# Kernel tuning notes

Hardware: AMD Instinct MI355X
Metric: run time of the kernel (lower is better)

The kernel has to match this reference:

```python
import jax, jax.numpy as jnp
import numpy as np
import math

N, S, T, E, H = 2, 2048, 2048, 1024, 16
HD = E // H  # head_dim = 64


def setup_inputs() -> dict:
    key = jax.random.key(0)
    ks = jax.random.split(key, 11)
    scale = 1.0 / math.sqrt(E)
    inp = {
        "query": jax.random.normal(ks[0], (N, S, E), jnp.float32),
        "key": jax.random.normal(ks[1], (N, T, E), jnp.float32),
        "value": jax.random.normal(ks[2], (N, T, E), jnp.float32),
        "Wq": jax.random.normal(ks[3], (E, E), jnp.float32) * scale,
        "bq": jnp.zeros((E,), jnp.float32),
        "Wk": jax.random.normal(ks[4], (E, E), jnp.float32) * scale,
        "bk": jnp.zeros((E,), jnp.float32),
        "Wv": jax.random.normal(ks[5], (E, E), jnp.float32) * scale,
        "bv": jnp.zeros((E,), jnp.float32),
        "Wo": jax.random.normal(ks[6], (E, E), jnp.float32) * scale,
        "bo": jnp.zeros((E,), jnp.float32),
    }
    return inp


def reference(query, key, value, Wq, bq, Wk, bk, Wv, bv, Wo, bo):
    # QKV projections, then split heads: [N, S, E] -> [N, H, S, HD]
    q = (query @ Wq + bq).reshape(N, S, H, HD).transpose(0, 2, 1, 3)
    k = (key @ Wk + bk).reshape(N, T, H, HD).transpose(0, 2, 1, 3)
    v = (value @ Wv + bv).reshape(N, T, H, HD).transpose(0, 2, 1, 3)
    # scaled dot-product attention scores [N, H, S, T]
    scores = jnp.einsum('nhse,nhte->nhst', q, k) / math.sqrt(HD)
    attn = jax.nn.softmax(scores, axis=-1)
    # dropout is identity in eval mode
    out = jnp.einsum('nhst,nhte->nhse', attn, v)  # [N, H, S, HD]
    out = out.transpose(0, 2, 1, 3).reshape(N, S, E)
    return out @ Wo + bo
```

## Files before the change

kernel.cpp:

```cpp
#include <hip/hip_runtime.h>
#include <hip/hip_bf16.h>

typedef __bf16 bf16x8 __attribute__((ext_vector_type(8)));
typedef __bf16 bf16x4 __attribute__((ext_vector_type(4)));
typedef float  f32x4  __attribute__((ext_vector_type(4)));
typedef float  f32x16 __attribute__((ext_vector_type(16)));
typedef unsigned int u32x4 __attribute__((ext_vector_type(4)));

#define MFMA16(a, b, c) __builtin_amdgcn_mfma_f32_16x16x32_bf16((a), (b), (c), 0, 0, 0)
#define MFMA32(a, b, c) __builtin_amdgcn_mfma_f32_32x32x16_bf16((a), (b), (c), 0, 0, 0)

constexpr int SEQ = 2048, EMB = 1024, NHEAD = 16, HD = 64;
constexpr float SSCALE = 0.18033688f;

__device__ __forceinline__ void glds16(const void* g, void* l) {
    __builtin_amdgcn_global_load_lds(
        (const __attribute__((address_space(1))) void*)g,
        (__attribute__((address_space(3))) void*)l, 16, 0, 0);
}

__global__ __launch_bounds__(256)
void prep(const float* __restrict__ W0, const float* __restrict__ W1,
          const float* __restrict__ W2, const float* __restrict__ W3,
          __bf16* __restrict__ T0, __bf16* __restrict__ T1,
          __bf16* __restrict__ T2, __bf16* __restrict__ T3,
          const float* __restrict__ X0, const float* __restrict__ X1,
          const float* __restrict__ X2, __bf16* __restrict__ Y0,
          __bf16* __restrict__ Y1, __bf16* __restrict__ Y2)
{
    __shared__ float tile[32][33];
    const int z = blockIdx.z;
    if (z < 4) {
        const float* W = (z==0) ? W0 : (z==1) ? W1 : (z==2) ? W2 : W3;
        __bf16*      T = (z==0) ? T0 : (z==1) ? T1 : (z==2) ? T2 : T3;
        const float s = (z == 0) ? SSCALE : 1.0f;
        const int kb = blockIdx.x * 32, nb = blockIdx.y * 32;
        const int c = threadIdx.x & 31, r0 = threadIdx.x >> 5;
#pragma unroll
        for (int i = 0; i < 4; ++i)
            tile[r0 + 8*i][c] = W[(size_t)(kb + r0 + 8*i)*1024 + nb + c];
        __syncthreads();
#pragma unroll
        for (int i = 0; i < 4; ++i)
            T[(size_t)(nb + r0 + 8*i)*1024 + kb + c] = (__bf16)(tile[c][r0 + 8*i] * s);
    } else {
        const float* X = (z==4) ? X0 : (z==5) ? X1 : X2;
        __bf16*      Y = (z==4) ? Y0 : (z==5) ? Y1 : Y2;
        const size_t base =
            ((size_t)(blockIdx.y * 32 + blockIdx.x) * 256 + threadIdx.x) * 16;
#pragma unroll
        for (int j = 0; j < 2; ++j) {
            const float4* s4 = (const float4*)(X + base + j*8);
            float4 f0 = s4[0], f1 = s4[1];
            bf16x8 v;
            v[0]=(__bf16)f0.x; v[1]=(__bf16)f0.y; v[2]=(__bf16)f0.z; v[3]=(__bf16)f0.w;
            v[4]=(__bf16)f1.x; v[5]=(__bf16)f1.y; v[6]=(__bf16)f1.z; v[7]=(__bf16)f1.w;
            *(bf16x8*)(Y + base + j*8) = v;
        }
    }
}

struct GArg { const __bf16* A; const __bf16* Bt; const float* bias; void* C;
              int mode; int kbase; int kcount; float bscale; };
struct GArgs3 { GArg a[3]; };

__global__ __launch_bounds__(256)
void gemmk(GArgs3 args)
{
    const int lin = blockIdx.x + (blockIdx.y << 5) + (blockIdx.z << 8);
    const int nid = (lin & 7) * 96 + (lin >> 3);
    const int gz = nid >> 8, rem = nid & 255;
    const int bm = rem >> 3, bn = rem & 7;
    const GArg g = args.a[gz];
    __shared__ __attribute__((aligned(16))) __bf16 As[128*64];
    __shared__ __attribute__((aligned(16))) __bf16 Bs[128*64];
    const int tid = threadIdx.x, lane = tid & 63, wave = tid >> 6;
    const int wm = wave >> 1, wn = wave & 1;
    const int quad = lane >> 4, l16 = lane & 15;

    f32x4 acc[4][4] = {};

    for (int kt = 0; kt < g.kcount; ++kt) {
        const int k0 = g.kbase + kt*64;
        __syncthreads();
#pragma unroll
        for (int j = 0; j < 4; ++j) {
            const int ci = j*256 + tid;
            const int row = ci >> 3, cg = ((ci & 7) ^ (row & 7)) * 8;
            glds16(g.A + (size_t)(bm*128 + row)*1024 + k0 + cg,
                   &As[(j*256 + wave*64)*8]);
        }
#pragma unroll
        for (int j = 0; j < 4; ++j) {
            const int ci = j*256 + tid;
            const int row = ci >> 3, cg = ((ci & 7) ^ (row & 7)) * 8;
            glds16(g.Bt + (size_t)(bn*128 + row)*1024 + k0 + cg,
                   &Bs[(j*256 + wave*64)*8]);
        }
        __syncthreads();
#pragma unroll
        for (int ks = 0; ks < 2; ++ks) {
            const int kc = ks*4 + quad;
            bf16x8 af[4], bfr[4];
#pragma unroll
            for (int mt = 0; mt < 4; ++mt) {
                const int ar = wm*64 + mt*16 + l16;
                af[mt] = *(const bf16x8*)&As[ar*64 + (kc ^ (ar & 7))*8];
            }
#pragma unroll
            for (int nt = 0; nt < 4; ++nt) {
                const int br = wn*64 + nt*16 + l16;
                bfr[nt] = *(const bf16x8*)&Bs[br*64 + (kc ^ (br & 7))*8];
            }
#pragma unroll
            for (int mt = 0; mt < 4; ++mt)
#pragma unroll
                for (int nt = 0; nt < 4; ++nt)
                    acc[mt][nt] = MFMA16(af[mt], bfr[nt], acc[mt][nt]);
        }
    }

#pragma unroll
    for (int nt = 0; nt < 4; ++nt) {
        const int n = bn*128 + wn*64 + nt*16 + l16;
        const float bvs = (g.bias ? g.bias[n] : 0.f) * g.bscale;
#pragma unroll
        for (int mt = 0; mt < 4; ++mt) {
            const int mbase = bm*128 + wm*64 + mt*16 + quad*4;
            f32x4 v = acc[mt][nt];
            if (g.mode == 0) {
                __bf16* C = (__bf16*)g.C;
                const int h = n >> 6, d = n & 63;
#pragma unroll
                for (int r = 0; r < 4; ++r) {
                    const int m = mbase + r;
                    const int nb = m >> 11, s = m & 2047;
                    C[(size_t)(nb*NHEAD + h)*(SEQ*HD) + (size_t)s*HD + d] = (__bf16)(v[r] + bvs);
                }
            } else {
                __bf16* C = (__bf16*)g.C;
                const int h = n >> 6, d = n & 63;
                const int nb = mbase >> 11, s = mbase & 2047;
                const int tg = (s >> 2) & 7;
                const int pg = (tg & 4) | ((tg & 1) << 1) | ((tg & 2) >> 1);
                const int sp = (s & ~31) | (pg << 2);
                bf16x4 o;
#pragma unroll
                for (int r = 0; r < 4; ++r) o[r] = (__bf16)(v[r] + bvs);
                *(bf16x4*)&C[(size_t)(nb*NHEAD + h)*(SEQ*HD) + (size_t)d*SEQ + sp] = o;
            }
        }
    }
}

__global__ __launch_bounds__(256)
void gemmo(const __bf16* __restrict__ A, const __bf16* __restrict__ Bt,
           const float* __restrict__ bias, float* __restrict__ C)
{
    const int lin = blockIdx.x + (blockIdx.y << 6);
    const int nid = (lin & 7) * 64 + (lin >> 3);
    const int bm = nid >> 3, bn = nid & 7;
    __shared__ __attribute__((aligned(16))) __bf16 As[64*64];
    __shared__ __attribute__((aligned(16))) __bf16 Bs[128*64];
    const int tid = threadIdx.x, lane = tid & 63, wave = tid >> 6;
    const int quad = lane >> 4, l16 = lane & 15;

    f32x4 acc[4][2] = {};

    for (int k0 = 0; k0 < 1024; k0 += 64) {
        __syncthreads();
#pragma unroll
        for (int j = 0; j < 2; ++j) {
            const int ci = j*256 + tid;
            const int row = ci >> 3, cg = ((ci & 7) ^ (row & 7)) * 8;
            glds16(A + (size_t)(bm*64 + row)*1024 + k0 + cg,
                   &As[(j*256 + wave*64)*8]);
        }
#pragma unroll
        for (int j = 0; j < 4; ++j) {
            const int ci = j*256 + tid;
            const int row = ci >> 3, cg = ((ci & 7) ^ (row & 7)) * 8;
            glds16(Bt + (size_t)(bn*128 + row)*1024 + k0 + cg,
                   &Bs[(j*256 + wave*64)*8]);
        }
        __syncthreads();
#pragma unroll
        for (int ks = 0; ks < 2; ++ks) {
            const int kc = ks*4 + quad;
            bf16x8 af[4], bfr[2];
#pragma unroll
            for (int mt = 0; mt < 4; ++mt) {
                const int ar = mt*16 + l16;
                af[mt] = *(const bf16x8*)&As[ar*64 + (kc ^ (ar & 7))*8];
            }
#pragma unroll
            for (int nt = 0; nt < 2; ++nt) {
                const int br = wave*32 + nt*16 + l16;
                bfr[nt] = *(const bf16x8*)&Bs[br*64 + (kc ^ (br & 7))*8];
            }
#pragma unroll
            for (int mt = 0; mt < 4; ++mt)
#pragma unroll
                for (int nt = 0; nt < 2; ++nt)
                    acc[mt][nt] = MFMA16(af[mt], bfr[nt], acc[mt][nt]);
        }
    }
#pragma unroll
    for (int nt = 0; nt < 2; ++nt) {
        const int n = bn*128 + wave*32 + nt*16 + l16;
        const float bv = bias[n];
#pragma unroll
        for (int mt = 0; mt < 4; ++mt) {
            const int mbase = bm*64 + mt*16 + quad*4;
            f32x4 v = acc[mt][nt];
#pragma unroll
            for (int r = 0; r < 4; ++r)
                C[(size_t)(mbase + r)*1024 + n] = v[r] + bv;
        }
    }
}

__global__ __launch_bounds__(512, 2)
void attn32(const __bf16* __restrict__ qg, const __bf16* __restrict__ kg,
            const __bf16* __restrict__ vg, __bf16* __restrict__ Og)
{
    __shared__ __attribute__((aligned(16))) char smem[64*1024];
    float* Xch = (float*)smem;

    const int tid = threadIdx.x, lane = tid & 63, wave = tid >> 6;
    const int w4 = wave & 3, grp = wave >> 2;
    const int l32 = lane & 31, half = lane >> 5;
    const int nh = blockIdx.y;
    const int q0 = blockIdx.x * 128;
    const __bf16* qb = qg + (size_t)nh * (SEQ*HD);
    const __bf16* kb = kg + (size_t)nh * (SEQ*HD);
    const __bf16* vb = vg + (size_t)nh * (SEQ*HD);

    bf16x8 qf[4];
#pragma unroll
    for (int ks = 0; ks < 4; ++ks)
        qf[ks] = *(const bf16x8*)(qb + (size_t)(q0 + w4*32 + l32)*HD + ks*16 + half*8);

    bf16x8 vone;
#pragma unroll
    for (int i = 0; i < 8; ++i) vone[i] = (__bf16)1.0f;

    f32x16 oacc[2] = {};
    f32x16 osum = {};

    const int cK0 = tid, rK0 = cK0 >> 3;
    const int cK1 = 512 + tid, rK1 = cK1 >> 3;
    const __bf16* kp0 = kb + (size_t)rK0*HD + ((cK0 & 7) ^ (rK0 & 7)) * 8;
    const __bf16* kp1 = kb + (size_t)rK1*HD + ((cK1 & 7) ^ (rK1 & 7)) * 8;
    const int cV0 = tid, rV0 = cV0 >> 4, pV0 = cV0 & 15;
    const int cV1 = 512 + tid, rV1 = cV1 >> 4, pV1 = cV1 & 15;
    const __bf16* vp0 = vb + (size_t)rV0*SEQ + (((pV0 & ~7) | ((pV0 & 7) ^ (rV0 & 7))) * 8);
    const __bf16* vp1 = vb + (size_t)rV1*SEQ + (((pV1 & ~7) | ((pV1 & 7) ^ (rV1 & 7))) * 8);

    auto stage = [&](int b) {
        char* Kd = smem + b * 16384;
        char* Vd = smem + 32768 + b * 16384;
        glds16(kp0, Kd + wave*1024);
        glds16(kp1, Kd + 8192 + wave*1024);
        glds16(vp0, Vd + wave*1024);
        glds16(vp1, Vd + 8192 + wave*1024);
        kp0 += 128*HD; kp1 += 128*HD;
        vp0 += 128;    vp1 += 128;
    };

    stage(0);
    int cur = 0;
    for (int it = 0; it < 16; ++it) {
        __syncthreads();
        if (it < 15) stage(cur ^ 1);

        const __bf16* Ks = (const __bf16*)(smem + cur * 16384);
        const __bf16* Vs = (const __bf16*)(smem + 32768 + cur * 16384);

        f32x16 sc[2] = {};
        __builtin_amdgcn_s_setprio(1);
#pragma unroll
        for (int ks = 0; ks < 4; ++ks) {
            const int c = ks*2 + half;
#pragma unroll
            for (int nt = 0; nt < 2; ++nt) {
                const int kr = grp*64 + nt*32 + l32;
                bf16x8 kf = *(const bf16x8*)&Ks[kr*64 + ((c ^ (kr & 7))*8)];
                sc[nt] = MFMA32(kf, qf[ks], sc[nt]);
            }
        }
        __builtin_amdgcn_s_setprio(0);

#pragma unroll
        for (int nt = 0; nt < 2; ++nt)
#pragma unroll
            for (int sub = 0; sub < 2; ++sub) {
                const float e0 = __builtin_amdgcn_exp2f(sc[nt][sub*8 + 0]);
                const float e1 = __builtin_amdgcn_exp2f(sc[nt][sub*8 + 1]);
                const float e2 = __builtin_amdgcn_exp2f(sc[nt][sub*8 + 2]);
                const float e3 = __builtin_amdgcn_exp2f(sc[nt][sub*8 + 3]);
                const float e4 = __builtin_amdgcn_exp2f(sc[nt][sub*8 + 4]);
                const float e5 = __builtin_amdgcn_exp2f(sc[nt][sub*8 + 5]);
                const float e6 = __builtin_amdgcn_exp2f(sc[nt][sub*8 + 6]);
                const float e7 = __builtin_amdgcn_exp2f(sc[nt][sub*8 + 7]);
                u32x4 pk;
                asm("v_cvt_pk_bf16_f32 %0, %1, %2" : "=v"(pk.x) : "v"(e0), "v"(e1));
                asm("v_cvt_pk_bf16_f32 %0, %1, %2" : "=v"(pk.y) : "v"(e2), "v"(e3));
                asm("v_cvt_pk_bf16_f32 %0, %1, %2" : "=v"(pk.z) : "v"(e4), "v"(e5));
                asm("v_cvt_pk_bf16_f32 %0, %1, %2" : "=v"(pk.w) : "v"(e6), "v"(e7));
                const bf16x8 pf = __builtin_bit_cast(bf16x8, pk);
                const int c2 = grp*8 + (nt*2 + sub)*2 + half;
                __builtin_amdgcn_s_setprio(1);
#pragma unroll
                for (int dt = 0; dt < 2; ++dt) {
                    const int vr = dt*32 + l32;
                    const int pos = (c2 & ~7) | ((c2 & 7) ^ (vr & 7));
                    bf16x8 vf = *(const bf16x8*)&Vs[vr*128 + pos*8];
                    oacc[dt] = MFMA32(pf, vf, oacc[dt]);
                }
                osum = MFMA32(pf, vone, osum);
                __builtin_amdgcn_s_setprio(0);
            }
        cur ^= 1;
    }

    __syncthreads();
    if (grp == 1) {
        float* dst = &Xch[((w4*64) + lane) * 48];
#pragma unroll
        for (int i = 0; i < 16; ++i) {
            dst[i]      = oacc[0][i];
            dst[16 + i] = oacc[1][i];
            dst[32 + i] = osum[i];
        }
    }
    __syncthreads();
    if (grp == 0) {
        const float* src = &Xch[((w4*64) + lane) * 48];
#pragma unroll
        for (int i = 0; i < 16; ++i) {
            oacc[0][i] += src[i];
            oacc[1][i] += src[16 + i];
            osum[i]    += src[32 + i];
        }
        const int nb = nh >> 4, h = nh & 15;
#pragma unroll
        for (int reg = 0; reg < 16; ++reg) {
            const int row = (reg & 3) + 8*(reg >> 2) + 4*half;
            const int srow = q0 + w4*32 + row;
            const float inv = 1.0f / osum[reg];
#pragma unroll
            for (int dt = 0; dt < 2; ++dt)
                Og[(size_t)(nb*SEQ + srow)*EMB + h*HD + dt*32 + l32] =
                    (__bf16)(oacc[dt][reg] * inv);
        }
    }
}

extern "C" void kernel_launch(void* const* d_in, const int* in_sizes, int n_in,
                              void* d_out, int out_size, void* d_ws, size_t ws_size,
                              hipStream_t stream)
{
    const float* query = (const float*)d_in[0];
    const float* key_  = (const float*)d_in[1];
    const float* value = (const float*)d_in[2];
    const float* Wq = (const float*)d_in[3];
    const float* bq = (const float*)d_in[4];
    const float* Wk = (const float*)d_in[5];
    const float* bk = (const float*)d_in[6];
    const float* Wv = (const float*)d_in[7];
    const float* bv = (const float*)d_in[8];
    const float* Wo = (const float*)d_in[9];
    const float* bo = (const float*)d_in[10];
    float* out = (float*)d_out;

    constexpr size_t SZW = 1024u*1024u;
    constexpr size_t SZX = 4096u*1024u;
    __bf16* ws  = (__bf16*)d_ws;
    __bf16* WqT = ws;
    __bf16* WkT = WqT + SZW;
    __bf16* WvT = WkT + SZW;
    __bf16* WoT = WvT + SZW;
    __bf16* xv  = WoT + SZW;
    __bf16* qh  = xv + SZX;
    __bf16* kh  = qh + SZX;
    __bf16* vTh = kh + SZX;
    __bf16* xq  = (__bf16*)d_out;
    __bf16* xk  = xq + SZX;
    __bf16* Oh  = xv;

    prep<<<dim3(32, 32, 7), 256, 0, stream>>>(Wq, Wk, Wv, Wo, WqT, WkT, WvT, WoT,
                                              query, key_, value, xq, xk, xv);
    GArgs3 a;
    a.a[0] = { xq, WqT, bq, qh,  0, 0, 16, SSCALE };
    a.a[1] = { xk, WkT, bk, kh,  0, 0, 16, 1.0f };
    a.a[2] = { xv, WvT, bv, vTh, 1, 0, 16, 1.0f };
    gemmk<<<dim3(32, 8, 3), 256, 0, stream>>>(a);
    attn32<<<dim3(16, 32), 512, 0, stream>>>(qh, kh, vTh, Oh);
    gemmo<<<dim3(64, 8), 256, 0, stream>>>(Oh, WoT, bo, out);
}
```

Measured before the change: 211.6 us.

## Software-pipeline QK and PV across iterations, replace ones-MFMA rowsum with scalar sums

```diff
diff --git a/kernel.cpp b/kernel.cpp
--- a/kernel.cpp
+++ b/kernel.cpp
@@ -224,7 +224,7 @@
 void attn32(const __bf16* __restrict__ qg, const __bf16* __restrict__ kg,
             const __bf16* __restrict__ vg, __bf16* __restrict__ Og)
 {
-    __shared__ __attribute__((aligned(16))) char smem[64*1024];
+    __shared__ __attribute__((aligned(16))) char smem[80*1024];
     float* Xch = (float*)smem;
 
     const int tid = threadIdx.x, lane = tid & 63, wave = tid >> 6;
@@ -241,12 +241,8 @@
     for (int ks = 0; ks < 4; ++ks)
         qf[ks] = *(const bf16x8*)(qb + (size_t)(q0 + w4*32 + l32)*HD + ks*16 + half*8);
 
-    bf16x8 vone;
-#pragma unroll
-    for (int i = 0; i < 8; ++i) vone[i] = (__bf16)1.0f;
-
     f32x16 oacc[2] = {};
-    f32x16 osum = {};
+    float psum = 0.0f;
 
     const int cK0 = tid, rK0 = cK0 >> 3;
     const int cK1 = 512 + tid, rK1 = cK1 >> 3;
@@ -257,9 +253,9 @@
     const __bf16* vp0 = vb + (size_t)rV0*SEQ + (((pV0 & ~7) | ((pV0 & 7) ^ (rV0 & 7))) * 8);
     const __bf16* vp1 = vb + (size_t)rV1*SEQ + (((pV1 & ~7) | ((pV1 & 7) ^ (rV1 & 7))) * 8);
 
-    auto stage = [&](int b) {
-        char* Kd = smem + b * 16384;
-        char* Vd = smem + 32768 + b * 16384;
+    auto stage = [&](int t) {
+        char* Kd = smem + (t & 1) * 16384;
+        char* Vd = smem + 32768 + (t % 3) * 16384;
         glds16(kp0, Kd + wave*1024);
         glds16(kp1, Kd + 8192 + wave*1024);
         glds16(vp0, Vd + wave*1024);
@@ -268,16 +264,8 @@
         vp0 += 128;    vp1 += 128;
     };
 
-    stage(0);
-    int cur = 0;
-    for (int it = 0; it < 16; ++it) {
-        __syncthreads();
-        if (it < 15) stage(cur ^ 1);
-
-        const __bf16* Ks = (const __bf16*)(smem + cur * 16384);
-        const __bf16* Vs = (const __bf16*)(smem + 32768 + cur * 16384);
-
-        f32x16 sc[2] = {};
+    auto qk = [&](const __bf16* Ks, f32x16* sc) {
+        sc[0] = (f32x16){}; sc[1] = (f32x16){};
         __builtin_amdgcn_s_setprio(1);
 #pragma unroll
         for (int ks = 0; ks < 4; ++ks) {
@@ -290,7 +278,9 @@
             }
         }
         __builtin_amdgcn_s_setprio(0);
-
+    };
+
+    auto epv = [&](const f32x16* sc, const __bf16* Vs) {
 #pragma unroll
         for (int nt = 0; nt < 2; ++nt)
 #pragma unroll
@@ -303,6 +293,7 @@
                 const float e5 = __builtin_amdgcn_exp2f(sc[nt][sub*8 + 5]);
                 const float e6 = __builtin_amdgcn_exp2f(sc[nt][sub*8 + 6]);
                 const float e7 = __builtin_amdgcn_exp2f(sc[nt][sub*8 + 7]);
+                psum += ((e0 + e1) + (e2 + e3)) + ((e4 + e5) + (e6 + e7));
                 u32x4 pk;
                 asm("v_cvt_pk_bf16_f32 %0, %1, %2" : "=v"(pk.x) : "v"(e0), "v"(e1));
                 asm("v_cvt_pk_bf16_f32 %0, %1, %2" : "=v"(pk.y) : "v"(e2), "v"(e3));
@@ -318,37 +309,54 @@
                     bf16x8 vf = *(const bf16x8*)&Vs[vr*128 + pos*8];
                     oacc[dt] = MFMA32(pf, vf, oacc[dt]);
                 }
-                osum = MFMA32(pf, vone, osum);
                 __builtin_amdgcn_s_setprio(0);
             }
-        cur ^= 1;
-    }
+    };
+
+    stage(0);
+    __syncthreads();
+    stage(1);
+    f32x16 scp[2];
+    qk((const __bf16*)smem, scp);
+
+    for (int it = 1; it < 16; ++it) {
+        __syncthreads();
+        if (it < 15) stage(it + 1);
+        f32x16 scn[2];
+        qk((const __bf16*)(smem + (it & 1) * 16384), scn);
+        epv(scp, (const __bf16*)(smem + 32768 + ((it - 1) % 3) * 16384));
+        scp[0] = scn[0]; scp[1] = scn[1];
+    }
+    epv(scp, (const __bf16*)(smem + 32768));
 
     __syncthreads();
     if (grp == 1) {
-        float* dst = &Xch[((w4*64) + lane) * 48];
+        float* dst = &Xch[((w4*64) + lane) * 33];
 #pragma unroll
         for (int i = 0; i < 16; ++i) {
             dst[i]      = oacc[0][i];
             dst[16 + i] = oacc[1][i];
-            dst[32 + i] = osum[i];
-        }
+        }
+        dst[32] = psum;
     }
     __syncthreads();
     if (grp == 0) {
-        const float* src = &Xch[((w4*64) + lane) * 48];
+        const float* src = &Xch[((w4*64) + lane) * 33];
 #pragma unroll
         for (int i = 0; i < 16; ++i) {
             oacc[0][i] += src[i];
             oacc[1][i] += src[16 + i];
-            osum[i]    += src[32 + i];
-        }
+        }
+        psum += src[32];
+        psum += __shfl(psum, lane ^ 32);
+        float* dl = (float*)(smem + 76*1024);
+        if (half == 0) dl[w4*32 + l32] = psum;
         const int nb = nh >> 4, h = nh & 15;
 #pragma unroll
         for (int reg = 0; reg < 16; ++reg) {
             const int row = (reg & 3) + 8*(reg >> 2) + 4*half;
             const int srow = q0 + w4*32 + row;
-            const float inv = 1.0f / osum[reg];
+            const float inv = 1.0f / dl[w4*32 + row];
 #pragma unroll
             for (int dt = 0; dt < 2; ++dt)
                 Og[(size_t)(nb*SEQ + srow)*EMB + h*HD + dt*32 + l32] =
```

New measurement: 215.3 us. About the same (+1.8%).
